# Kernel optimization log

Measured on AMD Instinct MI355X. Metric: run time of the kernel, lower is better.

Reference implementation:

```python
import jax, jax.numpy as jnp
import numpy as np

SEQ = 8192
EMB = 1024
MID = 1024


def setup_inputs() -> dict:
    key = jax.random.key(0)
    ks = jax.random.split(key, 7)
    s = 1.0 / np.sqrt(EMB)
    return {
        "text_encoded": jax.random.normal(ks[0], (SEQ, EMB), dtype=jnp.float32),
        "Wq": jax.random.normal(ks[1], (MID, EMB), dtype=jnp.float32) * s,
        "bq": jax.random.normal(ks[2], (MID,), dtype=jnp.float32) * 0.02,
        "Wk": jax.random.normal(ks[3], (MID, EMB), dtype=jnp.float32) * s,
        "bk": jax.random.normal(ks[4], (MID,), dtype=jnp.float32) * 0.02,
        "Wv": jax.random.normal(ks[5], (MID, EMB), dtype=jnp.float32) * s,
        "bv": jax.random.normal(ks[6], (MID,), dtype=jnp.float32) * 0.02,
    }


def reference(text_encoded, Wq, bq, Wk, bk, Wv, bv):
    # torch nn.Linear: y = x @ W.T + b, W is [out, in]
    Q = text_encoded @ Wq.T + bq  # [S, M]
    K = text_encoded @ Wk.T + bk  # [S, M]
    V = text_encoded @ Wv.T + bv  # [S, M]
    # cosine-similarity scores: (Q K^T) scaled by outer(1/||Q||, 1/||K||)
    inv_qn = jax.lax.rsqrt(jnp.sum(Q * Q, axis=1))  # [S]
    inv_kn = jax.lax.rsqrt(jnp.sum(K * K, axis=1))  # [S]
    scores = (Q @ K.T) * (inv_qn[:, None] * inv_kn[None, :])  # [S, S]
    weights = jax.nn.softmax(scores, axis=1)
    return weights @ V  # [S, M]
```

## Files before the change

### kernel.cpp

```cpp
#include <hip/hip_runtime.h>


#define SEQ 8192
#define MID 1024
#define EMB 1024

typedef __attribute__((ext_vector_type(8))) short short8x;
typedef __attribute__((ext_vector_type(16))) float float16x;
typedef __attribute__((ext_vector_type(4))) int int4x;
typedef __attribute__((ext_vector_type(16))) int int16x;

__device__ __forceinline__ unsigned short f2bf(float x) {
  union { float f; unsigned u; } v; v.f = x;
  unsigned r = v.u + 0x7FFFu + ((v.u >> 16) & 1u);
  return (unsigned short)(r >> 16);
}
__device__ __forceinline__ float bf2f(unsigned short h) {
  union { unsigned u; float f; } v; v.u = ((unsigned)h) << 16;
  return v.f;
}
__device__ __forceinline__ float fexp2(float x) {
#if __has_builtin(__builtin_amdgcn_exp2f)
  return __builtin_amdgcn_exp2f(x);
#else
  return __expf(x * 0.6931471805599453f);
#endif
}

__device__ __forceinline__ void g2l16(const void* g, void* lds) {
  __builtin_amdgcn_global_load_lds(
      (const __attribute__((address_space(1))) unsigned int*)g,
      (__attribute__((address_space(3))) unsigned int*)lds, 16, 0, 0);
}

__device__ __forceinline__ void gemm128_nt(
    const unsigned short* __restrict__ A, const unsigned short* __restrict__ B,
    long lda, long ldb, int m0, int n0, int K,
    unsigned short* As, unsigned short* Bs, float16x acc[2][2]) {
  const int tid = threadIdx.x;
  const int w = tid >> 6;
  const int l = tid & 63;
  const int wm = (w & 1) << 6;
  const int wn = (w >> 1) << 6;
  const int srow = l >> 3;
  const int skg = (l & 7) ^ srow;
  const int l31 = l & 31;
  const int lh = l >> 5;
  const int swz = l31 & 7;

  for (int k0 = 0; k0 < K; k0 += 64) {
    __syncthreads();
#pragma unroll
    for (int r = 0; r < 4; ++r) {
      const int rr = (w * 4 + r) * 8 + srow;
      g2l16(A + (long)(m0 + rr) * lda + k0 + skg * 8, As + (w * 4 + r) * 512);
      g2l16(B + (long)(n0 + rr) * ldb + k0 + skg * 8, Bs + (w * 4 + r) * 512);
    }
    __syncthreads();
#pragma unroll
    for (int ks = 0; ks < 4; ++ks) {
      const int kg = ks * 2 + lh;
      short8x av[2], bv[2];
#pragma unroll
      for (int t = 0; t < 2; ++t) {
        av[t] = *(const short8x*)(As + (wm + t * 32 + l31) * 64 + ((kg ^ swz) << 3));
        bv[t] = *(const short8x*)(Bs + (wn + t * 32 + l31) * 64 + ((kg ^ swz) << 3));
      }
#pragma unroll
      for (int tm = 0; tm < 2; ++tm)
#pragma unroll
        for (int tn = 0; tn < 2; ++tn)
          acc[tm][tn] = __builtin_amdgcn_mfma_f32_32x32x16_bf16(av[tm], bv[tn], acc[tm][tn], 0, 0, 0);
    }
  }
}

__device__ __forceinline__ void gemm128_nt_i8(
    const unsigned char* __restrict__ A, const unsigned char* __restrict__ B,
    long lda, long ldb, int m0, int n0, int Kbytes,
    unsigned char* As, unsigned char* Bs, int16x acc[2][2]) {
  const int tid = threadIdx.x;
  const int w = tid >> 6;
  const int l = tid & 63;
  const int wm = (w & 1) << 6;
  const int wn = (w >> 1) << 6;
  const int srow = l >> 3;
  const int skg = (l & 7) ^ srow;
  const int l31 = l & 31;
  const int lh = l >> 5;
  const int swz = l31 & 7;

  for (int k0 = 0; k0 < Kbytes; k0 += 128) {
    __syncthreads();
#pragma unroll
    for (int r = 0; r < 4; ++r) {
      const int rr = (w * 4 + r) * 8 + srow;
      g2l16(A + (long)(m0 + rr) * lda + k0 + skg * 16, As + (w * 4 + r) * 1024);
      g2l16(B + (long)(n0 + rr) * ldb + k0 + skg * 16, Bs + (w * 4 + r) * 1024);
    }
    __syncthreads();
#pragma unroll
    for (int ks = 0; ks < 4; ++ks) {
      const int kg = ks * 2 + lh;
      int4x av[2], bv[2];
#pragma unroll
      for (int t = 0; t < 2; ++t) {
        av[t] = *(const int4x*)(As + (wm + t * 32 + l31) * 128 + ((kg ^ swz) << 4));
        bv[t] = *(const int4x*)(Bs + (wn + t * 32 + l31) * 128 + ((kg ^ swz) << 4));
      }
#pragma unroll
      for (int tm = 0; tm < 2; ++tm)
#pragma unroll
        for (int tn = 0; tn < 2; ++tn)
          acc[tm][tn] = __builtin_amdgcn_mfma_i32_32x32x32_i8(av[tm], bv[tn], acc[tm][tn], 0, 0, 0);
    }
  }
}

__global__ void cvt_all(const float* __restrict__ X,
                        const float* __restrict__ wq, const float* __restrict__ wk,
                        const float* __restrict__ wv,
                        unsigned short* __restrict__ Xb, unsigned short* __restrict__ Wb,
                        float* __restrict__ sums) {
  const long i = ((long)blockIdx.x * 256 + threadIdx.x) * 4;
  if (i < 24576) *(float4*)(sums + i) = (float4){0.f, 0.f, 0.f, 0.f};
  const float* src;
  unsigned short* dst;
  long off;
  if (i < (long)SEQ * EMB) {
    src = X; dst = Xb; off = i;
  } else {
    long j = i - (long)SEQ * EMB;
    int t = (int)(j >> 20);
    off = j & (MID * EMB - 1);
    src = (t == 0) ? wq : (t == 1) ? wk : wv;
    dst = Wb + (long)t * MID * EMB;
  }
  float4 v = *(const float4*)(src + off);
  ushort4 o;
  o.x = f2bf(v.x); o.y = f2bf(v.y); o.z = f2bf(v.z); o.w = f2bf(v.w);
  *(ushort4*)(dst + off) = o;
}

__global__ __launch_bounds__(256) void qkv_kernel(
    const unsigned short* __restrict__ Xb, const unsigned short* __restrict__ Wb,
    const float* __restrict__ bq, const float* __restrict__ bk, const float* __restrict__ bv,
    unsigned char* __restrict__ Q8, unsigned char* __restrict__ K8,
    unsigned char* __restrict__ VT8, float* __restrict__ sumsq) {
  __shared__ unsigned short smem[16384];
  unsigned short* As = smem;
  unsigned short* Bs = smem + 8192;
  const int z = blockIdx.z;
  const int m0 = blockIdx.y * 128;
  const int n0 = blockIdx.x * 128;
  float16x acc[2][2];
#pragma unroll
  for (int i = 0; i < 2; ++i)
#pragma unroll
    for (int j = 0; j < 2; ++j)
#pragma unroll
      for (int e = 0; e < 16; ++e) acc[i][j][e] = 0.f;

  gemm128_nt(Xb, Wb + (long)z * MID * EMB, EMB, EMB, m0, n0, EMB, As, Bs, acc);

  const int tid = threadIdx.x;
  const int l = tid & 63, w = tid >> 6;
  const int wm = (w & 1) << 6, wn = (w >> 1) << 6;
  const int l31 = l & 31, lh = l >> 5;
  const float* bias = (z == 0) ? bq : (z == 1) ? bk : bv;
  float bvv[2];
#pragma unroll
  for (int tn = 0; tn < 2; ++tn) bvv[tn] = bias[n0 + wn + tn * 32 + l31];
#pragma unroll
  for (int tm = 0; tm < 2; ++tm)
#pragma unroll
    for (int tn = 0; tn < 2; ++tn)
#pragma unroll
      for (int r = 0; r < 16; ++r) acc[tm][tn][r] += bvv[tn];

  __syncthreads();

  if (z < 2) {
#pragma unroll
    for (int tm = 0; tm < 2; ++tm)
#pragma unroll
      for (int tn = 0; tn < 2; ++tn) {
        const int rcol = wn + tn * 32 + l31;
#pragma unroll
        for (int r = 0; r < 16; ++r) {
          float v = acc[tm][tn][r];
          float po = __shfl_xor(v, 1);
          if (!(l & 1)) {
            const int rrow = wm + tm * 32 + (r & 3) + 8 * (r >> 2) + 4 * lh;
            const int chunk = (rcol >> 3) ^ (rrow & 7);
            unsigned pk = (unsigned)f2bf(v) | ((unsigned)f2bf(po) << 16);
            *(unsigned*)(smem + rrow * 128 + (chunk << 3) + (rcol & 7)) = pk;
          }
        }
      }
    __syncthreads();
    unsigned char* O8 = z ? K8 : Q8;
    float* ss = sumsq + (long)z * SEQ;
    const float qs = 127.0f / 8.0f;
#pragma unroll
    for (int round = 0; round < 8; ++round) {
      const int row = round * 16 + (tid >> 4);
      const int c = tid & 15;
      short8x vv = *(const short8x*)(smem + row * 128 + ((c ^ (row & 7)) << 3));
      int qq[8];
      float s = 0.f;
#pragma unroll
      for (int j = 0; j < 8; ++j) {
        float t = rintf(bf2f((unsigned short)vv[j]) * qs);
        t = fminf(127.f, fmaxf(-127.f, t));
        qq[j] = (int)t;
        s += t * t;
      }
      unsigned lo = (qq[0] & 255) | ((qq[1] & 255) << 8) | ((qq[2] & 255) << 16) | ((qq[3] & 255) << 24);
      unsigned hi = (qq[4] & 255) | ((qq[5] & 255) << 8) | ((qq[6] & 255) << 16) | ((qq[7] & 255) << 24);
      int2 pk; pk.x = (int)lo; pk.y = (int)hi;
      *(int2*)(O8 + (long)(m0 + row) * MID + n0 + c * 8) = pk;
      s += __shfl_xor(s, 1); s += __shfl_xor(s, 2);
      s += __shfl_xor(s, 4); s += __shfl_xor(s, 8);
      if (c == 0) atomicAdd(ss + m0 + row, s);
    }
  } else {
#pragma unroll
    for (int tm = 0; tm < 2; ++tm)
#pragma unroll
      for (int tn = 0; tn < 2; ++tn) {
        const int nn = wn + tn * 32 + l31;
#pragma unroll
        for (int g = 0; g < 4; ++g) {
          const int mm = wm + tm * 32 + 8 * g + 4 * lh;
          const int chunk = (mm >> 3) ^ (nn & 7);
          ushort4 pk;
          pk.x = f2bf(acc[tm][tn][g * 4 + 0]);
          pk.y = f2bf(acc[tm][tn][g * 4 + 1]);
          pk.z = f2bf(acc[tm][tn][g * 4 + 2]);
          pk.w = f2bf(acc[tm][tn][g * 4 + 3]);
          *(ushort4*)(smem + nn * 128 + (chunk << 3) + (mm & 7)) = pk;
        }
      }
    __syncthreads();
    const float vs = 127.0f / 6.0f;
#pragma unroll
    for (int round = 0; round < 8; ++round) {
      const int nn = round * 16 + (tid >> 4);
      const int c = tid & 15;
      short8x vv = *(const short8x*)(smem + nn * 128 + ((c ^ (nn & 7)) << 3));
      int qq[8];
#pragma unroll
      for (int j = 0; j < 8; ++j) {
        float t = rintf(bf2f((unsigned short)vv[j]) * vs);
        t = fminf(127.f, fmaxf(-127.f, t));
        qq[j] = (int)t;
      }
      unsigned lo = (qq[0] & 255) | ((qq[1] & 255) << 8) | ((qq[2] & 255) << 16) | ((qq[3] & 255) << 24);
      unsigned hi = (qq[4] & 255) | ((qq[5] & 255) << 8) | ((qq[6] & 255) << 16) | ((qq[7] & 255) << 24);
      int2 pk; pk.x = (int)lo; pk.y = (int)hi;
      *(int2*)(VT8 + (long)(n0 + nn) * SEQ + m0 + c * 8) = pk;
    }
  }
}

__global__ __launch_bounds__(256, 4) void score_kernel(
    const unsigned char* __restrict__ Q8, const unsigned char* __restrict__ K8,
    const float* __restrict__ sumsq,
    unsigned char* __restrict__ P8, float* __restrict__ denomq) {
  __shared__ unsigned short smem[16384];
  unsigned char* As = (unsigned char*)smem;
  unsigned char* Bs = (unsigned char*)smem + 16384;
  const int m0 = blockIdx.y * 128;
  const int n0 = blockIdx.x * 128;
  int16x acc[2][2];
#pragma unroll
  for (int i = 0; i < 2; ++i)
#pragma unroll
    for (int j = 0; j < 2; ++j)
#pragma unroll
      for (int e = 0; e < 16; ++e) acc[i][j][e] = 0;

  gemm128_nt_i8(K8, Q8, MID, MID, n0, m0, MID, As, Bs, acc);

  const int tid = threadIdx.x;
  const int l = tid & 63, w = tid >> 6;
  const int wm = (w & 1) << 6, wn = (w >> 1) << 6;
  const int l31 = l & 31, lh = l >> 5;

  const float LOG2E  = 1.4426950408889634f;
  const float LOG2PS = 5.5459896458832860f;
  const float MAGIC  = 12582912.0f;
  float qi[2];
#pragma unroll
  for (int tn = 0; tn < 2; ++tn)
    qi[tn] = rsqrtf(sumsq[m0 + wn + tn * 32 + l31]) * LOG2E;

  __syncthreads();

  unsigned char* Plds = As;
#pragma unroll
  for (int tm = 0; tm < 2; ++tm) {
#pragma unroll
    for (int g = 0; g < 4; ++g) {
      const int nb = wm + tm * 32 + g * 8 + lh * 4;
      float4 ss4 = *(const float4*)(sumsq + SEQ + n0 + nb);
      float ik0 = rsqrtf(ss4.x), ik1 = rsqrtf(ss4.y);
      float ik2 = rsqrtf(ss4.z), ik3 = rsqrtf(ss4.w);
#pragma unroll
      for (int tn = 0; tn < 2; ++tn) {
        unsigned u0 = __float_as_uint(fexp2(fmaf((float)acc[tm][tn][g * 4 + 0] * ik0, qi[tn], LOG2PS)) + MAGIC);
        unsigned u1 = __float_as_uint(fexp2(fmaf((float)acc[tm][tn][g * 4 + 1] * ik1, qi[tn], LOG2PS)) + MAGIC);
        unsigned u2 = __float_as_uint(fexp2(fmaf((float)acc[tm][tn][g * 4 + 2] * ik2, qi[tn], LOG2PS)) + MAGIC);
        unsigned u3 = __float_as_uint(fexp2(fmaf((float)acc[tm][tn][g * 4 + 3] * ik3, qi[tn], LOG2PS)) + MAGIC);
        unsigned pk = (u0 & 255) | ((u1 & 255) << 8) | ((u2 & 255) << 16) | (u3 << 24);
        const int ml = wn + tn * 32 + l31;
        const int addr = ml * 128 + ((((nb >> 4) ^ (ml & 7)) << 4) | (nb & 15));
        *(unsigned*)(Plds + addr) = pk;
      }
    }
  }
  __syncthreads();

  const unsigned M8 = 0x00FF00FFu;
#pragma unroll
  for (int round = 0; round < 4; ++round) {
    const int row = round * 32 + (tid >> 3);
    const int c = tid & 7;
    const int addr = row * 128 + ((c ^ (row & 7)) << 4);
    uint4 v = *(const uint4*)(Plds + addr);
    unsigned e = (v.x & M8) + (v.y & M8) + (v.z & M8) + (v.w & M8);
    unsigned o = ((v.x >> 8) & M8) + ((v.y >> 8) & M8) + ((v.z >> 8) & M8) + ((v.w >> 8) & M8);
    unsigned t = e + o;
    unsigned s = (t & 0xFFFFu) + (t >> 16);
    *(uint4*)(P8 + (long)(m0 + row) * SEQ + n0 + c * 16) = v;
    s += __shfl_xor(s, 1); s += __shfl_xor(s, 2); s += __shfl_xor(s, 4);
    if (c == 0) atomicAdd(denomq + m0 + row, (float)s);
  }
}

__global__ __launch_bounds__(256, 4) void out_kernel(
    const unsigned char* __restrict__ P8, const unsigned char* __restrict__ VT8,
    const float* __restrict__ denomq, float* __restrict__ out) {
  __shared__ unsigned char smem8[32768];
  unsigned char* As = smem8;
  unsigned char* Bs = smem8 + 16384;
  const int n0 = blockIdx.x * 128;
  const int m0 = blockIdx.y * 128;
  int16x acc[2][2];
#pragma unroll
  for (int i = 0; i < 2; ++i)
#pragma unroll
    for (int j = 0; j < 2; ++j)
#pragma unroll
      for (int e = 0; e < 16; ++e) acc[i][j][e] = 0;

  gemm128_nt_i8(P8, VT8, SEQ, SEQ, m0, n0, SEQ, As, Bs, acc);

  const int l = threadIdx.x & 63, w = threadIdx.x >> 6;
  const int wm = (w & 1) << 6, wn = (w >> 1) << 6;
  const int l31 = l & 31, lh = l >> 5;
  const float sv = 127.0f / 6.0f;
#pragma unroll
  for (int tm = 0; tm < 2; ++tm)
#pragma unroll
    for (int r = 0; r < 16; ++r) {
      const int row = m0 + wm + tm * 32 + (r & 3) + 8 * (r >> 2) + 4 * lh;
      const float inv = 1.0f / (sv * denomq[row]);
#pragma unroll
      for (int tn = 0; tn < 2; ++tn) {
        const int col = n0 + wn + tn * 32 + l31;
        out[(long)row * MID + col] = (float)acc[tm][tn][r] * inv;
      }
    }
}

extern "C" void kernel_launch(void* const* d_in, const int* in_sizes, int n_in,
                              void* d_out, int out_size, void* d_ws, size_t ws_size,
                              hipStream_t stream) {
  const float* X  = (const float*)d_in[0];
  const float* Wq = (const float*)d_in[1];
  const float* bq = (const float*)d_in[2];
  const float* Wk = (const float*)d_in[3];
  const float* bk = (const float*)d_in[4];
  const float* Wv = (const float*)d_in[5];
  const float* bv = (const float*)d_in[6];

  char* wsb = (char*)d_ws;
  const size_t MB = 1ull << 20;
  unsigned char* Q8  = (unsigned char*)(wsb);
  unsigned char* K8  = (unsigned char*)(wsb + 8 * MB);
  unsigned char* VT8 = (unsigned char*)(wsb + 16 * MB);
  float* sums        = (float*)(wsb + 24 * MB);
  float* denomq      = sums + 2 * SEQ;
  unsigned char* P8  = (unsigned char*)(wsb + 25 * MB);
  unsigned short* Xb = (unsigned short*)(wsb + 25 * MB);
  unsigned short* Wb = (unsigned short*)(wsb + 41 * MB);

  const int cvt_elems = SEQ * EMB + 3 * MID * EMB;
  cvt_all<<<cvt_elems / 1024, 256, 0, stream>>>(X, Wq, Wk, Wv, Xb, Wb, sums);

  qkv_kernel<<<dim3(MID / 128, SEQ / 128, 3), 256, 0, stream>>>(Xb, Wb, bq, bk, bv, Q8, K8, VT8, sums);
  score_kernel<<<dim3(SEQ / 128, SEQ / 128), 256, 0, stream>>>(Q8, K8, sums, P8, denomq);
  out_kernel<<<dim3(MID / 128, SEQ / 128), 256, 0, stream>>>(P8, VT8, denomq, (float*)d_out);
}
```

Measured before the change: 334.5 us.

## Enlarge int8 GEMM tiles to 256x128 in score and output kernels

Replaces the 128x128 int8 MFMA tile with a 256x128 tile so each wave computes a 128x64 sub-tile, raising operand reuse per LDS/global load. The score kernel's P staging layout and swizzle are widened to 256-byte rows and the row-sum reduction is extended across 16 lanes. Launch bounds drop to 2 blocks per CU and grids shrink, which reduces occupancy and, for the output kernel, leaves only about one block per CU.

```diff
diff --git a/kernel.cpp b/kernel.cpp
--- a/kernel.cpp
+++ b/kernel.cpp
@@ -75,14 +75,14 @@
   }
 }
 
-__device__ __forceinline__ void gemm128_nt_i8(
+__device__ __forceinline__ void gemm256x128_nt_i8(
     const unsigned char* __restrict__ A, const unsigned char* __restrict__ B,
     long lda, long ldb, int m0, int n0, int Kbytes,
-    unsigned char* As, unsigned char* Bs, int16x acc[2][2]) {
+    unsigned char* As, unsigned char* Bs, int16x acc[4][2]) {
   const int tid = threadIdx.x;
   const int w = tid >> 6;
   const int l = tid & 63;
-  const int wm = (w & 1) << 6;
+  const int wm = (w & 1) << 7;
   const int wn = (w >> 1) << 6;
   const int srow = l >> 3;
   const int skg = (l & 7) ^ srow;
@@ -93,23 +93,28 @@
   for (int k0 = 0; k0 < Kbytes; k0 += 128) {
     __syncthreads();
 #pragma unroll
+    for (int r = 0; r < 8; ++r) {
+      const int rr = (w * 8 + r) * 8 + srow;
+      g2l16(A + (long)(m0 + rr) * lda + k0 + skg * 16, As + (w * 8 + r) * 1024);
+    }
+#pragma unroll
     for (int r = 0; r < 4; ++r) {
       const int rr = (w * 4 + r) * 8 + srow;
-      g2l16(A + (long)(m0 + rr) * lda + k0 + skg * 16, As + (w * 4 + r) * 1024);
       g2l16(B + (long)(n0 + rr) * ldb + k0 + skg * 16, Bs + (w * 4 + r) * 1024);
     }
     __syncthreads();
 #pragma unroll
     for (int ks = 0; ks < 4; ++ks) {
       const int kg = ks * 2 + lh;
-      int4x av[2], bv[2];
-#pragma unroll
-      for (int t = 0; t < 2; ++t) {
+      int4x av[4], bv[2];
+#pragma unroll
+      for (int t = 0; t < 4; ++t)
         av[t] = *(const int4x*)(As + (wm + t * 32 + l31) * 128 + ((kg ^ swz) << 4));
+#pragma unroll
+      for (int t = 0; t < 2; ++t)
         bv[t] = *(const int4x*)(Bs + (wn + t * 32 + l31) * 128 + ((kg ^ swz) << 4));
-      }
-#pragma unroll
-      for (int tm = 0; tm < 2; ++tm)
+#pragma unroll
+      for (int tm = 0; tm < 4; ++tm)
 #pragma unroll
         for (int tn = 0; tn < 2; ++tn)
           acc[tm][tn] = __builtin_amdgcn_mfma_i32_32x32x32_i8(av[tm], bv[tn], acc[tm][tn], 0, 0, 0);
@@ -264,28 +269,28 @@
   }
 }
 
-__global__ __launch_bounds__(256, 4) void score_kernel(
+__global__ __launch_bounds__(256, 2) void score_kernel(
     const unsigned char* __restrict__ Q8, const unsigned char* __restrict__ K8,
     const float* __restrict__ sumsq,
     unsigned char* __restrict__ P8, float* __restrict__ denomq) {
-  __shared__ unsigned short smem[16384];
-  unsigned char* As = (unsigned char*)smem;
-  unsigned char* Bs = (unsigned char*)smem + 16384;
-  const int m0 = blockIdx.y * 128;
-  const int n0 = blockIdx.x * 128;
-  int16x acc[2][2];
-#pragma unroll
-  for (int i = 0; i < 2; ++i)
+  __shared__ unsigned char smem8[49152];
+  unsigned char* As = smem8;
+  unsigned char* Bs = smem8 + 32768;
+  const int kb0 = blockIdx.x * 256;
+  const int qb0 = blockIdx.y * 128;
+  int16x acc[4][2];
+#pragma unroll
+  for (int i = 0; i < 4; ++i)
 #pragma unroll
     for (int j = 0; j < 2; ++j)
 #pragma unroll
       for (int e = 0; e < 16; ++e) acc[i][j][e] = 0;
 
-  gemm128_nt_i8(K8, Q8, MID, MID, n0, m0, MID, As, Bs, acc);
+  gemm256x128_nt_i8(K8, Q8, MID, MID, kb0, qb0, MID, As, Bs, acc);
 
   const int tid = threadIdx.x;
   const int l = tid & 63, w = tid >> 6;
-  const int wm = (w & 1) << 6, wn = (w >> 1) << 6;
+  const int wm = (w & 1) << 7, wn = (w >> 1) << 6;
   const int l31 = l & 31, lh = l >> 5;
 
   const float LOG2E  = 1.4426950408889634f;
@@ -294,17 +299,17 @@
   float qi[2];
 #pragma unroll
   for (int tn = 0; tn < 2; ++tn)
-    qi[tn] = rsqrtf(sumsq[m0 + wn + tn * 32 + l31]) * LOG2E;
+    qi[tn] = rsqrtf(sumsq[qb0 + wn + tn * 32 + l31]) * LOG2E;
 
   __syncthreads();
 
   unsigned char* Plds = As;
 #pragma unroll
-  for (int tm = 0; tm < 2; ++tm) {
+  for (int tm = 0; tm < 4; ++tm) {
 #pragma unroll
     for (int g = 0; g < 4; ++g) {
       const int nb = wm + tm * 32 + g * 8 + lh * 4;
-      float4 ss4 = *(const float4*)(sumsq + SEQ + n0 + nb);
+      float4 ss4 = *(const float4*)(sumsq + SEQ + kb0 + nb);
       float ik0 = rsqrtf(ss4.x), ik1 = rsqrtf(ss4.y);
       float ik2 = rsqrtf(ss4.z), ik3 = rsqrtf(ss4.w);
 #pragma unroll
@@ -315,7 +320,7 @@
         unsigned u3 = __float_as_uint(fexp2(fmaf((float)acc[tm][tn][g * 4 + 3] * ik3, qi[tn], LOG2PS)) + MAGIC);
         unsigned pk = (u0 & 255) | ((u1 & 255) << 8) | ((u2 & 255) << 16) | (u3 << 24);
         const int ml = wn + tn * 32 + l31;
-        const int addr = ml * 128 + ((((nb >> 4) ^ (ml & 7)) << 4) | (nb & 15));
+        const int addr = ml * 256 + ((((nb >> 4) ^ (ml & 15)) << 4) | (nb & 15));
         *(unsigned*)(Plds + addr) = pk;
       }
     }
@@ -324,45 +329,46 @@
 
   const unsigned M8 = 0x00FF00FFu;
 #pragma unroll
-  for (int round = 0; round < 4; ++round) {
-    const int row = round * 32 + (tid >> 3);
-    const int c = tid & 7;
-    const int addr = row * 128 + ((c ^ (row & 7)) << 4);
+  for (int round = 0; round < 8; ++round) {
+    const int row = round * 16 + (tid >> 4);
+    const int c = tid & 15;
+    const int addr = row * 256 + ((c ^ (row & 15)) << 4);
     uint4 v = *(const uint4*)(Plds + addr);
     unsigned e = (v.x & M8) + (v.y & M8) + (v.z & M8) + (v.w & M8);
     unsigned o = ((v.x >> 8) & M8) + ((v.y >> 8) & M8) + ((v.z >> 8) & M8) + ((v.w >> 8) & M8);
     unsigned t = e + o;
     unsigned s = (t & 0xFFFFu) + (t >> 16);
-    *(uint4*)(P8 + (long)(m0 + row) * SEQ + n0 + c * 16) = v;
-    s += __shfl_xor(s, 1); s += __shfl_xor(s, 2); s += __shfl_xor(s, 4);
-    if (c == 0) atomicAdd(denomq + m0 + row, (float)s);
-  }
-}
-
-__global__ __launch_bounds__(256, 4) void out_kernel(
+    *(uint4*)(P8 + (long)(qb0 + row) * SEQ + kb0 + c * 16) = v;
+    s += __shfl_xor(s, 1); s += __shfl_xor(s, 2);
+    s += __shfl_xor(s, 4); s += __shfl_xor(s, 8);
+    if (c == 0) atomicAdd(denomq + qb0 + row, (float)s);
+  }
+}
+
+__global__ __launch_bounds__(256, 2) void out_kernel(
     const unsigned char* __restrict__ P8, const unsigned char* __restrict__ VT8,
     const float* __restrict__ denomq, float* __restrict__ out) {
-  __shared__ unsigned char smem8[32768];
+  __shared__ unsigned char smem8[49152];
   unsigned char* As = smem8;
-  unsigned char* Bs = smem8 + 16384;
+  unsigned char* Bs = smem8 + 32768;
   const int n0 = blockIdx.x * 128;
-  const int m0 = blockIdx.y * 128;
-  int16x acc[2][2];
-#pragma unroll
-  for (int i = 0; i < 2; ++i)
+  const int m0 = blockIdx.y * 256;
+  int16x acc[4][2];
+#pragma unroll
+  for (int i = 0; i < 4; ++i)
 #pragma unroll
     for (int j = 0; j < 2; ++j)
 #pragma unroll
       for (int e = 0; e < 16; ++e) acc[i][j][e] = 0;
 
-  gemm128_nt_i8(P8, VT8, SEQ, SEQ, m0, n0, SEQ, As, Bs, acc);
+  gemm256x128_nt_i8(P8, VT8, SEQ, SEQ, m0, n0, SEQ, As, Bs, acc);
 
   const int l = threadIdx.x & 63, w = threadIdx.x >> 6;
-  const int wm = (w & 1) << 6, wn = (w >> 1) << 6;
+  const int wm = (w & 1) << 7, wn = (w >> 1) << 6;
   const int l31 = l & 31, lh = l >> 5;
   const float sv = 127.0f / 6.0f;
 #pragma unroll
-  for (int tm = 0; tm < 2; ++tm)
+  for (int tm = 0; tm < 4; ++tm)
 #pragma unroll
     for (int r = 0; r < 16; ++r) {
       const int row = m0 + wm + tm * 32 + (r & 3) + 8 * (r >> 2) + 4 * lh;
@@ -401,6 +407,6 @@
   cvt_all<<<cvt_elems / 1024, 256, 0, stream>>>(X, Wq, Wk, Wv, Xb, Wb, sums);
 
   qkv_kernel<<<dim3(MID / 128, SEQ / 128, 3), 256, 0, stream>>>(Xb, Wb, bq, bk, bv, Q8, K8, VT8, sums);
-  score_kernel<<<dim3(SEQ / 128, SEQ / 128), 256, 0, stream>>>(Q8, K8, sums, P8, denomq);
-  out_kernel<<<dim3(MID / 128, SEQ / 128), 256, 0, stream>>>(P8, VT8, denomq, (float*)d_out);
-}
+  score_kernel<<<dim3(SEQ / 256, SEQ / 128), 256, 0, stream>>>(Q8, K8, sums, P8, denomq);
+  out_kernel<<<dim3(MID / 128, SEQ / 256), 256, 0, stream>>>(P8, VT8, denomq, (float*)d_out);
+}
```

Measured after the change: 374.2 us. 11.9% more time.
